# Optimization experiments

Measured on AMD Instinct MI355X. Metric: run time of the kernel, lower is better.

## Reference

```python
import jax, jax.numpy as jnp
import numpy as np

DIM = 256
NH = 8
HD = DIM // NH          # 32
KD = HD // 2            # 16, attn_ratio=0.5
SCALE = KD ** -0.5
EPS = 1e-3              # BatchNorm2d eps=0.001
B, H, W = 8, 32, 32


def _bn(x, g, b, m, v):
    # inference-mode BatchNorm2d over channel axis 1 of NCHW
    inv = g / jnp.sqrt(v + EPS)
    return x * inv[None, :, None, None] + (b - m * inv)[None, :, None, None]


def setup_inputs() -> dict:
    key = jax.random.key(0)
    ks = jax.random.split(key, 16)
    h_out = DIM + 2 * NH * KD  # 512
    return {
        "x": jax.random.normal(ks[0], (B, DIM, H, W), jnp.float32),
        "qkv_w": jax.random.normal(ks[1], (h_out, DIM), jnp.float32) * 0.05,
        "qkv_g": jax.random.uniform(ks[2], (h_out,), jnp.float32, 0.5, 1.5),
        "qkv_b": jax.random.normal(ks[3], (h_out,), jnp.float32) * 0.1,
        "qkv_m": jax.random.normal(ks[4], (h_out,), jnp.float32) * 0.1,
        "qkv_v": jax.random.uniform(ks[5], (h_out,), jnp.float32, 0.5, 1.5),
        "pe_w": jax.random.normal(ks[6], (DIM, 1, 3, 3), jnp.float32) * 0.1,
        "pe_g": jax.random.uniform(ks[7], (DIM,), jnp.float32, 0.5, 1.5),
        "pe_b": jax.random.normal(ks[8], (DIM,), jnp.float32) * 0.1,
        "pe_m": jax.random.normal(ks[9], (DIM,), jnp.float32) * 0.1,
        "pe_v": jax.random.uniform(ks[10], (DIM,), jnp.float32, 0.5, 1.5),
        "proj_w": jax.random.normal(ks[11], (DIM, DIM), jnp.float32) * 0.05,
        "proj_g": jax.random.uniform(ks[12], (DIM,), jnp.float32, 0.5, 1.5),
        "proj_b": jax.random.normal(ks[13], (DIM,), jnp.float32) * 0.1,
        "proj_m": jax.random.normal(ks[14], (DIM,), jnp.float32) * 0.1,
        "proj_v": jax.random.uniform(ks[15], (DIM,), jnp.float32, 0.5, 1.5),
    }


def reference(x, qkv_w, qkv_g, qkv_b, qkv_m, qkv_v,
              pe_w, pe_g, pe_b, pe_m, pe_v,
              proj_w, proj_g, proj_b, proj_m, proj_v):
    b, c, h, w = x.shape
    n = h * w
    # qkv: 1x1 conv (no bias) + BN, act=Identity
    qkv = _bn(jnp.einsum('oc,bchw->bohw', qkv_w, x), qkv_g, qkv_b, qkv_m, qkv_v)
    qkv = qkv.reshape(b, NH, 2 * KD + HD, n)
    q, k, v = jnp.split(qkv, [KD, 2 * KD], axis=2)  # [b,nh,kd,n],[b,nh,kd,n],[b,nh,hd,n]
    # attn = q^T @ k * scale, softmax over keys (last dim)
    attn = jax.nn.softmax(jnp.einsum('bhkn,bhkm->bhnm', q, k) * SCALE, axis=-1)
    # v @ attn^T -> [b,nh,hd,n]
    out = jnp.einsum('bhdj,bhij->bhdi', v, attn).reshape(b, c, h, w)
    # depthwise 3x3 positional branch on v (reshaped to spatial)
    v_sp = v.reshape(b, c, h, w)
    pe = jax.lax.conv_general_dilated(v_sp, pe_w, window_strides=(1, 1),
                                      padding=((1, 1), (1, 1)),
                                      feature_group_count=c)
    pe = _bn(pe, pe_g, pe_b, pe_m, pe_v)
    x_attn = out + pe
    # final 1x1 projection + BN
    return _bn(jnp.einsum('oc,bchw->bohw', proj_w, x_attn),
               proj_g, proj_b, proj_m, proj_v)
```

## Files before the change

### kernel.cpp

```cpp
#include <hip/hip_runtime.h>
#include <hip/hip_bf16.h>

#define B_    8
#define DIM_  256
#define NH_   8
#define HD_   32
#define KD_   16
#define HOUT_ 512
#define N_    1024
#define SCALE_ 0.25f
#define EPS_  1e-3f

typedef unsigned short u16;
typedef __attribute__((ext_vector_type(8))) short short8;
typedef __attribute__((ext_vector_type(4))) float f32x4;

union H4 { uint2 u; u16 e[4]; };

__device__ __forceinline__ float b2f(u16 u) {
    union { unsigned int i; float f; } c;
    c.i = ((unsigned int)u) << 16;
    return c.f;
}

__device__ __forceinline__ u16 f2b(float f) {
    union { float f; unsigned int i; } c;
    c.f = f;
    unsigned int x = c.i;
    return (u16)((x + 0x7fffu + ((x >> 16) & 1u)) >> 16);
}

__global__ __launch_bounds__(256) void k_prep(
    const float* __restrict__ qw, const float* __restrict__ pw,
    const float* __restrict__ pew,
    const float* __restrict__ qg, const float* __restrict__ qb,
    const float* __restrict__ qm, const float* __restrict__ qv,
    const float* __restrict__ pg, const float* __restrict__ pb,
    const float* __restrict__ pm, const float* __restrict__ pv,
    const float* __restrict__ eg, const float* __restrict__ eb,
    const float* __restrict__ em, const float* __restrict__ ev,
    u16* __restrict__ wq_bf, u16* __restrict__ wp_bf,
    float2* __restrict__ bnq, float2* __restrict__ bnp,
    float* __restrict__ wpe, float* __restrict__ bnpe)
{
    int i = blockIdx.x * 256 + threadIdx.x;
    wq_bf[i] = f2b(qw[i]);
    if (i < 65536) wp_bf[i] = f2b(pw[i]);
    if (i < 512) {
        float inv = qg[i] / sqrtf(qv[i] + EPS_);
        bnq[i] = make_float2(inv, qb[i] - qm[i] * inv);
    } else if (i < 768) {
        int o = i - 512;
        float inv = pg[o] / sqrtf(pv[o] + EPS_);
        bnp[o] = make_float2(inv, pb[o] - pm[o] * inv);
    }
    if (i < 2304) {
        int c = i / 9;
        float inv = eg[c] / sqrtf(ev[c] + EPS_);
        wpe[i] = pew[i] * inv;
        if (i % 9 == 0) bnpe[c] = eb[c] - em[c] * inv;
    }
}

__global__ __launch_bounds__(256) void k_xt(
    const float* __restrict__ x, u16* __restrict__ xT)
{
    __shared__ float t_s[64][65];
    int blk = blockIdx.x;
    int nt = blk & 15, ct = (blk >> 4) & 3, b = blk >> 6;
    int t = threadIdx.x;
    int c0 = ct * 64, n0 = nt * 64;
    #pragma unroll
    for (int i = 0; i < 16; ++i) {
        int idx = i * 256 + t;
        int c = idx >> 6, n = idx & 63;
        t_s[n][c] = x[(size_t)(b * DIM_ + c0 + c) * N_ + n0 + n];
    }
    __syncthreads();
    #pragma unroll
    for (int i = 0; i < 16; ++i) {
        int idx = i * 256 + t;
        int n = idx >> 6, c = idx & 63;
        xT[(size_t)(b * N_ + n0 + n) * DIM_ + c0 + c] = f2b(t_s[n][c]);
    }
}

__global__ __launch_bounds__(256) void k_qkv(
    const u16* __restrict__ xT, const u16* __restrict__ wbf,
    const float2* __restrict__ bn, u16* __restrict__ qkv)
{
    int blk = blockIdx.x;
    int nb = blk & 7, ob = (blk >> 3) & 7, b = blk >> 6;
    int t = threadIdx.x;
    int wv_ = t >> 6, lane = t & 63, quad = lane >> 4, l16 = lane & 15;
    int o_base = ob * 64 + (wv_ & 1) * 32;
    int n_base = nb * 128 + (wv_ >> 1) * 64;

    f32x4 acc[2][4];
    #pragma unroll
    for (int ot = 0; ot < 2; ++ot)
        #pragma unroll
        for (int nt = 0; nt < 4; ++nt) acc[ot][nt] = (f32x4){0.f, 0.f, 0.f, 0.f};

    const u16* xb = xT + (size_t)b * N_ * DIM_;
    for (int c0 = 0; c0 < DIM_; c0 += 32) {
        short8 af[2];
        #pragma unroll
        for (int ot = 0; ot < 2; ++ot)
            af[ot] = *(const short8*)(wbf + (size_t)(o_base + ot * 16 + l16) * DIM_ + c0 + quad * 8);
        short8 bf[4];
        #pragma unroll
        for (int nt = 0; nt < 4; ++nt)
            bf[nt] = *(const short8*)(xb + (size_t)(n_base + nt * 16 + l16) * DIM_ + c0 + quad * 8);
        #pragma unroll
        for (int ot = 0; ot < 2; ++ot)
            #pragma unroll
            for (int nt = 0; nt < 4; ++nt)
                acc[ot][nt] = __builtin_amdgcn_mfma_f32_16x16x32_bf16(af[ot], bf[nt], acc[ot][nt], 0, 0, 0);
    }
    #pragma unroll
    for (int ot = 0; ot < 2; ++ot)
        #pragma unroll
        for (int r = 0; r < 4; ++r) {
            int o = o_base + ot * 16 + quad * 4 + r;
            float2 ib = bn[o];
            u16* dst = qkv + (size_t)(b * HOUT_ + o) * N_ + n_base + l16;
            #pragma unroll
            for (int nt = 0; nt < 4; ++nt)
                dst[nt * 16] = f2b(acc[ot][nt][r] * ib.x + ib.y);
        }
}

struct MainSmem { u16 k_t[256][24]; u16 p_s[4][16][80]; };
union  SmemU    { MainSmem m; float v_pe[128][33]; };

__global__ __launch_bounds__(256) void k_attn(
    const u16* __restrict__ qkv, const float* __restrict__ wpe,
    const float* __restrict__ bnpe, u16* __restrict__ xattnT)
{
    __shared__ SmemU su;
    __shared__ u16   q_t[64][24];
    __shared__ float o_s[4][32][17];

    int blk = blockIdx.x;
    int qb = blk & 15;
    int h  = (blk >> 4) & 7;
    int b  = blk >> 7;
    int t    = threadIdx.x;
    int wv_  = t >> 6;
    int lane = t & 63;
    int quad = lane >> 4;
    int l16  = lane & 15;
    const u16* base = qkv + (size_t)(b * HOUT_ + h * 64) * N_;

    {
        int q = t & 63, d4 = (t >> 6) * 4;
        H4 hh;
        #pragma unroll
        for (int i = 0; i < 4; ++i)
            hh.e[i] = f2b(b2f(base[(size_t)(d4 + i) * N_ + qb * 64 + q]) * SCALE_);
        *(uint2*)&q_t[q][d4] = hh.u;
    }
    __syncthreads();

    short8 qf = {0, 0, 0, 0, 0, 0, 0, 0};
    if (quad < 2) qf = *(const short8*)&q_t[wv_ * 16 + l16][quad * 8];

    f32x4 oa0 = {0.f, 0.f, 0.f, 0.f};
    f32x4 oa1 = {0.f, 0.f, 0.f, 0.f};
    float l_acc[4] = {0.f, 0.f, 0.f, 0.f};

    for (int ch = 0; ch < 4; ++ch) {
        int ch0 = ch * 256;
        __syncthreads();
        {
            #pragma unroll
            for (int d4 = 0; d4 < 16; d4 += 4) {
                H4 hh;
                #pragma unroll
                for (int i = 0; i < 4; ++i)
                    hh.e[i] = base[(size_t)(16 + d4 + i) * N_ + ch0 + t];
                *(uint2*)&su.m.k_t[t][d4] = hh.u;
            }
        }
        __syncthreads();

        for (int kt = 0; kt < 4; ++kt) {
            int key0 = ch0 + kt * 64;
            #pragma unroll
            for (int nt = 0; nt < 4; ++nt) {
                short8 kf = {0, 0, 0, 0, 0, 0, 0, 0};
                if (quad < 2) kf = *(const short8*)&su.m.k_t[kt * 64 + nt * 16 + l16][quad * 8];
                f32x4 zero = {0.f, 0.f, 0.f, 0.f};
                f32x4 s = __builtin_amdgcn_mfma_f32_16x16x32_bf16(qf, kf, zero, 0, 0, 0);
                #pragma unroll
                for (int r = 0; r < 4; ++r) {
                    float p = __expf(fminf(s[r], 80.f));
                    l_acc[r] += p;
                    su.m.p_s[wv_][quad * 4 + r][nt * 16 + l16] = f2b(p);
                }
            }
            #pragma unroll
            for (int kc = 0; kc < 2; ++kc) {
                short8 pf = *(const short8*)&su.m.p_s[wv_][l16][kc * 32 + quad * 8];
                {
                    const u16* vsrc = base + (size_t)(32 + l16) * N_ + key0 + kc * 32 + quad * 8;
                    oa0 = __builtin_amdgcn_mfma_f32_16x16x32_bf16(pf, *(const short8*)vsrc, oa0, 0, 0, 0);
                }
                {
                    const u16* vsrc = base + (size_t)(48 + l16) * N_ + key0 + kc * 32 + quad * 8;
                    oa1 = __builtin_amdgcn_mfma_f32_16x16x32_bf16(pf, *(const short8*)vsrc, oa1, 0, 0, 0);
                }
            }
        }
    }

    #pragma unroll
    for (int r = 0; r < 4; ++r) {
        float v = l_acc[r];
        v += __shfl_xor(v, 1);
        v += __shfl_xor(v, 2);
        v += __shfl_xor(v, 4);
        v += __shfl_xor(v, 8);
        l_acc[r] = v;
    }
    #pragma unroll
    for (int r = 0; r < 4; ++r) {
        o_s[wv_][l16][quad * 4 + r]      = oa0[r] / l_acc[r];
        o_s[wv_][16 + l16][quad * 4 + r] = oa1[r] / l_acc[r];
    }
    __syncthreads();

    {
        int ybase = qb * 2 - 1;
        #pragma unroll
        for (int i = 0; i < 16; ++i) {
            int idx = i * 256 + t;
            int d = idx >> 7, px = idx & 127;
            int y = ybase + (px >> 5);
            float v = 0.f;
            if (y >= 0 && y < 32)
                v = b2f(base[(size_t)(32 + d) * N_ + y * 32 + (px & 31)]);
            su.v_pe[px][d] = v;
        }
    }
    __syncthreads();

    {
        int d = t & 31, pxg = t >> 5;
        int c = h * 32 + d;
        float w9[9];
        #pragma unroll
        for (int k = 0; k < 9; ++k) w9[k] = wpe[c * 9 + k];
        float beta = bnpe[c];
        #pragma unroll
        for (int ii = 0; ii < 8; ++ii) {
            int pl = pxg * 8 + ii;
            int xx0 = pl & 31;
            float s = beta;
            #pragma unroll
            for (int dy = -1; dy <= 1; ++dy) {
                #pragma unroll
                for (int dx = -1; dx <= 1; ++dx) {
                    int xx = xx0 + dx;
                    if (xx < 0 || xx > 31) continue;
                    s += w9[(dy + 1) * 3 + (dx + 1)] * su.v_pe[pl + 32 + dy * 32 + dx][d];
                }
            }
            float o = o_s[pl >> 4][d][pl & 15];
            xattnT[(size_t)(b * N_ + qb * 64 + pl) * DIM_ + c] = f2b(o + s);
        }
    }
}

__global__ __launch_bounds__(256) void k_proj(
    const u16* __restrict__ xattnT, const u16* __restrict__ wbf,
    const float2* __restrict__ bn, float* __restrict__ out)
{
    int blk = blockIdx.x;
    int nb = blk & 7, ob = (blk >> 3) & 3, b = blk >> 5;
    int t = threadIdx.x;
    int wv_ = t >> 6, lane = t & 63, quad = lane >> 4, l16 = lane & 15;
    int o_base = ob * 64 + (wv_ & 1) * 32;
    int n_base = nb * 128 + (wv_ >> 1) * 64;

    f32x4 acc[2][4];
    #pragma unroll
    for (int ot = 0; ot < 2; ++ot)
        #pragma unroll
        for (int nt = 0; nt < 4; ++nt) acc[ot][nt] = (f32x4){0.f, 0.f, 0.f, 0.f};

    const u16* xb = xattnT + (size_t)b * N_ * DIM_;
    for (int c0 = 0; c0 < DIM_; c0 += 32) {
        short8 af[2];
        #pragma unroll
        for (int ot = 0; ot < 2; ++ot)
            af[ot] = *(const short8*)(wbf + (size_t)(o_base + ot * 16 + l16) * DIM_ + c0 + quad * 8);
        short8 bf[4];
        #pragma unroll
        for (int nt = 0; nt < 4; ++nt)
            bf[nt] = *(const short8*)(xb + (size_t)(n_base + nt * 16 + l16) * DIM_ + c0 + quad * 8);
        #pragma unroll
        for (int ot = 0; ot < 2; ++ot)
            #pragma unroll
            for (int nt = 0; nt < 4; ++nt)
                acc[ot][nt] = __builtin_amdgcn_mfma_f32_16x16x32_bf16(af[ot], bf[nt], acc[ot][nt], 0, 0, 0);
    }
    #pragma unroll
    for (int ot = 0; ot < 2; ++ot)
        #pragma unroll
        for (int r = 0; r < 4; ++r) {
            int o = o_base + ot * 16 + quad * 4 + r;
            float2 ib = bn[o];
            float* dst = out + (size_t)(b * DIM_ + o) * N_ + n_base + l16;
            #pragma unroll
            for (int nt = 0; nt < 4; ++nt)
                dst[nt * 16] = acc[ot][nt][r] * ib.x + ib.y;
        }
}

extern "C" void kernel_launch(void* const* d_in, const int* in_sizes, int n_in,
                              void* d_out, int out_size, void* d_ws, size_t ws_size,
                              hipStream_t stream)
{
    const float* x      = (const float*)d_in[0];
    const float* qkv_w  = (const float*)d_in[1];
    const float* qkv_g  = (const float*)d_in[2];
    const float* qkv_b  = (const float*)d_in[3];
    const float* qkv_m  = (const float*)d_in[4];
    const float* qkv_v  = (const float*)d_in[5];
    const float* pe_w   = (const float*)d_in[6];
    const float* pe_g   = (const float*)d_in[7];
    const float* pe_b   = (const float*)d_in[8];
    const float* pe_m   = (const float*)d_in[9];
    const float* pe_v   = (const float*)d_in[10];
    const float* proj_w = (const float*)d_in[11];
    const float* proj_g = (const float*)d_in[12];
    const float* proj_b = (const float*)d_in[13];
    const float* proj_m = (const float*)d_in[14];
    const float* proj_v = (const float*)d_in[15];
    float* out = (float*)d_out;

    char* p = (char*)d_ws;
    u16*    qkv    = (u16*)p;    p += (size_t)B_ * HOUT_ * N_ * sizeof(u16);
    u16*    xT     = (u16*)p;    p += (size_t)B_ * N_ * DIM_ * sizeof(u16);
    u16*    xattnT = (u16*)p;    p += (size_t)B_ * N_ * DIM_ * sizeof(u16);
    u16*    wq_bf  = (u16*)p;    p += (size_t)HOUT_ * DIM_ * sizeof(u16);
    u16*    wp_bf  = (u16*)p;    p += (size_t)DIM_ * DIM_ * sizeof(u16);
    float2* bnq    = (float2*)p; p += 512 * sizeof(float2);
    float2* bnp    = (float2*)p; p += 256 * sizeof(float2);
    float*  wpe    = (float*)p;  p += 2304 * sizeof(float);
    float*  bnpe   = (float*)p;

    hipLaunchKernelGGL(k_prep, dim3(512), dim3(256), 0, stream,
                       qkv_w, proj_w, pe_w,
                       qkv_g, qkv_b, qkv_m, qkv_v,
                       proj_g, proj_b, proj_m, proj_v,
                       pe_g, pe_b, pe_m, pe_v,
                       wq_bf, wp_bf, bnq, bnp, wpe, bnpe);
    hipLaunchKernelGGL(k_xt, dim3(512), dim3(256), 0, stream, x, xT);
    hipLaunchKernelGGL(k_qkv, dim3(512), dim3(256), 0, stream,
                       xT, wq_bf, bnq, qkv);
    hipLaunchKernelGGL(k_attn, dim3(B_ * NH_ * 16), dim3(256), 0, stream,
                       qkv, wpe, bnpe, xattnT);
    hipLaunchKernelGGL(k_proj, dim3(256), dim3(256), 0, stream,
                       xattnT, wp_bf, bnp, out);
}
```

Before: 159.5 us.

## Rework attention with 32x32 MFMA and register P, fuse prep kernels, retile proj

Attention now computes S^T with 32x32x16 MFMAs and keeps P in registers, exchanging halves across the wave with a lane shuffle instead of staging through LDS. The four waves are split into two key halves and two query tiles, and the partial outputs and row sums are merged in shared memory in the epilogue. This removes the wasted half-K 16x16 MFMA and the LDS round trip for P. The prep and transpose kernels are merged into one launch, and the projection uses smaller tiles for twice as many blocks. Partial outputs are rounded to bf16 before the merge, which costs some precision.

After: 152.1 us. 1.05x faster.

```diff
diff --git a/kernel.cpp b/kernel.cpp
--- a/kernel.cpp
+++ b/kernel.cpp
@@ -12,10 +12,13 @@
 #define EPS_  1e-3f
 
 typedef unsigned short u16;
-typedef __attribute__((ext_vector_type(8))) short short8;
-typedef __attribute__((ext_vector_type(4))) float f32x4;
+typedef unsigned int   u32;
+typedef __attribute__((ext_vector_type(8)))  short short8;
+typedef __attribute__((ext_vector_type(4)))  float f32x4;
+typedef __attribute__((ext_vector_type(16))) float f32x16;
 
 union H4 { uint2 u; u16 e[4]; };
+union FragU { uint4 u; short8 s; };
 
 __device__ __forceinline__ float b2f(u16 u) {
     union { unsigned int i; float f; } c;
@@ -30,7 +33,8 @@
     return (u16)((x + 0x7fffu + ((x >> 16) & 1u)) >> 16);
 }
 
-__global__ __launch_bounds__(256) void k_prep(
+__global__ __launch_bounds__(256) void k_pre(
+    const float* __restrict__ x, u16* __restrict__ xT,
     const float* __restrict__ qw, const float* __restrict__ pw,
     const float* __restrict__ pew,
     const float* __restrict__ qg, const float* __restrict__ qb,
@@ -43,32 +47,30 @@
     float2* __restrict__ bnq, float2* __restrict__ bnp,
     float* __restrict__ wpe, float* __restrict__ bnpe)
 {
-    int i = blockIdx.x * 256 + threadIdx.x;
-    wq_bf[i] = f2b(qw[i]);
-    if (i < 65536) wp_bf[i] = f2b(pw[i]);
-    if (i < 512) {
-        float inv = qg[i] / sqrtf(qv[i] + EPS_);
-        bnq[i] = make_float2(inv, qb[i] - qm[i] * inv);
-    } else if (i < 768) {
-        int o = i - 512;
-        float inv = pg[o] / sqrtf(pv[o] + EPS_);
-        bnp[o] = make_float2(inv, pb[o] - pm[o] * inv);
-    }
-    if (i < 2304) {
-        int c = i / 9;
-        float inv = eg[c] / sqrtf(ev[c] + EPS_);
-        wpe[i] = pew[i] * inv;
-        if (i % 9 == 0) bnpe[c] = eb[c] - em[c] * inv;
-    }
-}
-
-__global__ __launch_bounds__(256) void k_xt(
-    const float* __restrict__ x, u16* __restrict__ xT)
-{
     __shared__ float t_s[64][65];
     int blk = blockIdx.x;
+    int t = threadIdx.x;
+    if (blk >= 512) {
+        int i = (blk - 512) * 256 + t;
+        wq_bf[i] = f2b(qw[i]);
+        if (i < 65536) wp_bf[i] = f2b(pw[i]);
+        if (i < 512) {
+            float inv = qg[i] / sqrtf(qv[i] + EPS_);
+            bnq[i] = make_float2(inv, qb[i] - qm[i] * inv);
+        } else if (i < 768) {
+            int o = i - 512;
+            float inv = pg[o] / sqrtf(pv[o] + EPS_);
+            bnp[o] = make_float2(inv, pb[o] - pm[o] * inv);
+        }
+        if (i < 2304) {
+            int c = i / 9;
+            float inv = eg[c] / sqrtf(ev[c] + EPS_);
+            wpe[i] = pew[i] * inv;
+            if (i % 9 == 0) bnpe[c] = eb[c] - em[c] * inv;
+        }
+        return;
+    }
     int nt = blk & 15, ct = (blk >> 4) & 3, b = blk >> 6;
-    int t = threadIdx.x;
     int c0 = ct * 64, n0 = nt * 64;
     #pragma unroll
     for (int i = 0; i < 16; ++i) {
@@ -131,17 +133,15 @@
         }
 }
 
-struct MainSmem { u16 k_t[256][24]; u16 p_s[4][16][80]; };
-union  SmemU    { MainSmem m; float v_pe[128][33]; };
+struct MainS { u16 q_t[64][24]; u16 k_t[2][256][24]; };
+struct EpiS  { u16 o_acc[2][32][66]; float l_s[2][64]; float v_pe[128][33]; };
+union  SmemU { MainS m; EpiS e; };
 
 __global__ __launch_bounds__(256) void k_attn(
     const u16* __restrict__ qkv, const float* __restrict__ wpe,
     const float* __restrict__ bnpe, u16* __restrict__ xattnT)
 {
     __shared__ SmemU su;
-    __shared__ u16   q_t[64][24];
-    __shared__ float o_s[4][32][17];
-
     int blk = blockIdx.x;
     int qb = blk & 15;
     int h  = (blk >> 4) & 7;
@@ -149,88 +149,90 @@
     int t    = threadIdx.x;
     int wv_  = t >> 6;
     int lane = t & 63;
-    int quad = lane >> 4;
-    int l16  = lane & 15;
+    int q5   = lane & 31;
+    int hw   = lane >> 5;
+    int kh   = wv_ >> 1;
+    int qt   = wv_ & 1;
     const u16* base = qkv + (size_t)(b * HOUT_ + h * 64) * N_;
+    int q0g = qb * 64;
 
     {
         int q = t & 63, d4 = (t >> 6) * 4;
         H4 hh;
         #pragma unroll
         for (int i = 0; i < 4; ++i)
-            hh.e[i] = f2b(b2f(base[(size_t)(d4 + i) * N_ + qb * 64 + q]) * SCALE_);
-        *(uint2*)&q_t[q][d4] = hh.u;
+            hh.e[i] = f2b(b2f(base[(size_t)(d4 + i) * N_ + q0g + q]) * SCALE_);
+        *(uint2*)&su.m.q_t[q][d4] = hh.u;
     }
     __syncthreads();
 
-    short8 qf = {0, 0, 0, 0, 0, 0, 0, 0};
-    if (quad < 2) qf = *(const short8*)&q_t[wv_ * 16 + l16][quad * 8];
-
-    f32x4 oa0 = {0.f, 0.f, 0.f, 0.f};
-    f32x4 oa1 = {0.f, 0.f, 0.f, 0.f};
-    float l_acc[4] = {0.f, 0.f, 0.f, 0.f};
-
-    for (int ch = 0; ch < 4; ++ch) {
-        int ch0 = ch * 256;
+    short8 qf = *(const short8*)&su.m.q_t[qt * 32 + q5][hw * 8];
+
+    f32x16 oacc = {0.f,0.f,0.f,0.f, 0.f,0.f,0.f,0.f, 0.f,0.f,0.f,0.f, 0.f,0.f,0.f,0.f};
+    float l_lane = 0.f;
+
+    for (int ch = 0; ch < 2; ++ch) {
         __syncthreads();
         {
             #pragma unroll
-            for (int d4 = 0; d4 < 16; d4 += 4) {
-                H4 hh;
+            for (int s2 = 0; s2 < 2; ++s2) {
+                int key = s2 * 512 + ch * 256 + t;
                 #pragma unroll
-                for (int i = 0; i < 4; ++i)
-                    hh.e[i] = base[(size_t)(16 + d4 + i) * N_ + ch0 + t];
-                *(uint2*)&su.m.k_t[t][d4] = hh.u;
-            }
-        }
-        __syncthreads();
-
-        for (int kt = 0; kt < 4; ++kt) {
-            int key0 = ch0 + kt * 64;
-            #pragma unroll
-            for (int nt = 0; nt < 4; ++nt) {
-                short8 kf = {0, 0, 0, 0, 0, 0, 0, 0};
-                if (quad < 2) kf = *(const short8*)&su.m.k_t[kt * 64 + nt * 16 + l16][quad * 8];
-                f32x4 zero = {0.f, 0.f, 0.f, 0.f};
-                f32x4 s = __builtin_amdgcn_mfma_f32_16x16x32_bf16(qf, kf, zero, 0, 0, 0);
-                #pragma unroll
-                for (int r = 0; r < 4; ++r) {
-                    float p = __expf(fminf(s[r], 80.f));
-                    l_acc[r] += p;
-                    su.m.p_s[wv_][quad * 4 + r][nt * 16 + l16] = f2b(p);
+                for (int d4 = 0; d4 < 16; d4 += 4) {
+                    H4 hh;
+                    #pragma unroll
+                    for (int i = 0; i < 4; ++i)
+                        hh.e[i] = base[(size_t)(16 + d4 + i) * N_ + key];
+                    *(uint2*)&su.m.k_t[s2][t][d4] = hh.u;
                 }
             }
-            #pragma unroll
-            for (int kc = 0; kc < 2; ++kc) {
-                short8 pf = *(const short8*)&su.m.p_s[wv_][l16][kc * 32 + quad * 8];
-                {
-                    const u16* vsrc = base + (size_t)(32 + l16) * N_ + key0 + kc * 32 + quad * 8;
-                    oa0 = __builtin_amdgcn_mfma_f32_16x16x32_bf16(pf, *(const short8*)vsrc, oa0, 0, 0, 0);
-                }
-                {
-                    const u16* vsrc = base + (size_t)(48 + l16) * N_ + key0 + kc * 32 + quad * 8;
-                    oa1 = __builtin_amdgcn_mfma_f32_16x16x32_bf16(pf, *(const short8*)vsrc, oa1, 0, 0, 0);
-                }
+        }
+        __syncthreads();
+
+        #pragma unroll 2
+        for (int tile = 0; tile < 8; ++tile) {
+            int key0 = kh * 512 + ch * 256 + tile * 32;
+            short8 kf = *(const short8*)&su.m.k_t[kh][tile * 32 + q5][hw * 8];
+            f32x16 z = {0.f,0.f,0.f,0.f, 0.f,0.f,0.f,0.f, 0.f,0.f,0.f,0.f, 0.f,0.f,0.f,0.f};
+            f32x16 sT = __builtin_amdgcn_mfma_f32_32x32x16_bf16(kf, qf, z, 0, 0, 0);
+            u32 pk[8];
+            #pragma unroll
+            for (int j = 0; j < 8; ++j) {
+                float p0 = __expf(fminf(sT[2 * j], 80.f));
+                float p1 = __expf(fminf(sT[2 * j + 1], 80.f));
+                l_lane += p0 + p1;
+                pk[j] = (u32)f2b(p0) | ((u32)f2b(p1) << 16);
             }
-        }
-    }
-
-    #pragma unroll
-    for (int r = 0; r < 4; ++r) {
-        float v = l_acc[r];
-        v += __shfl_xor(v, 1);
-        v += __shfl_xor(v, 2);
-        v += __shfl_xor(v, 4);
-        v += __shfl_xor(v, 8);
-        l_acc[r] = v;
-    }
-    #pragma unroll
-    for (int r = 0; r < 4; ++r) {
-        o_s[wv_][l16][quad * 4 + r]      = oa0[r] / l_acc[r];
-        o_s[wv_][16 + l16][quad * 4 + r] = oa1[r] / l_acc[r];
-    }
+            #pragma unroll
+            for (int s = 0; s < 2; ++s) {
+                u32 s0 = hw ? pk[4 * s + 0] : pk[4 * s + 2];
+                u32 s1 = hw ? pk[4 * s + 1] : pk[4 * s + 3];
+                u32 r0 = __shfl_xor(s0, 32);
+                u32 r1 = __shfl_xor(s1, 32);
+                FragU pf;
+                pf.u.x = hw ? r0 : pk[4 * s + 0];
+                pf.u.y = hw ? r1 : pk[4 * s + 1];
+                pf.u.z = hw ? pk[4 * s + 2] : r0;
+                pf.u.w = hw ? pk[4 * s + 3] : r1;
+                const u16* vsrc = base + (size_t)(32 + q5) * N_ + key0 + s * 16 + hw * 8;
+                short8 vf = *(const short8*)vsrc;
+                oacc = __builtin_amdgcn_mfma_f32_32x32x16_bf16(vf, pf.s, oacc, 0, 0, 0);
+            }
+        }
+    }
+
+    float l_q = l_lane + __shfl_xor(l_lane, 32);
     __syncthreads();
 
+    {
+        int qg = qt * 32 + q5;
+        #pragma unroll
+        for (int r = 0; r < 16; ++r) {
+            int d = (r & 3) + 8 * (r >> 2) + 4 * hw;
+            su.e.o_acc[kh][d][qg] = f2b(oacc[r]);
+        }
+        if (hw == 0) su.e.l_s[kh][qg] = l_q;
+    }
     {
         int ybase = qb * 2 - 1;
         #pragma unroll
@@ -241,7 +243,7 @@
             float v = 0.f;
             if (y >= 0 && y < 32)
                 v = b2f(base[(size_t)(32 + d) * N_ + y * 32 + (px & 31)]);
-            su.v_pe[px][d] = v;
+            su.e.v_pe[px][d] = v;
         }
     }
     __syncthreads();
@@ -264,11 +266,12 @@
                 for (int dx = -1; dx <= 1; ++dx) {
                     int xx = xx0 + dx;
                     if (xx < 0 || xx > 31) continue;
-                    s += w9[(dy + 1) * 3 + (dx + 1)] * su.v_pe[pl + 32 + dy * 32 + dx][d];
+                    s += w9[(dy + 1) * 3 + (dx + 1)] * su.e.v_pe[pl + 32 + dy * 32 + dx][d];
                 }
             }
-            float o = o_s[pl >> 4][d][pl & 15];
-            xattnT[(size_t)(b * N_ + qb * 64 + pl) * DIM_ + c] = f2b(o + s);
+            float o = b2f(su.e.o_acc[0][d][pl]) + b2f(su.e.o_acc[1][d][pl]);
+            float l = su.e.l_s[0][pl] + su.e.l_s[1][pl];
+            xattnT[(size_t)(b * N_ + q0g + pl) * DIM_ + c] = f2b(o / fmaxf(l, 1e-30f) + s);
         }
     }
 }
@@ -278,17 +281,17 @@
     const float2* __restrict__ bn, float* __restrict__ out)
 {
     int blk = blockIdx.x;
-    int nb = blk & 7, ob = (blk >> 3) & 3, b = blk >> 5;
+    int nb = blk & 15, ob = (blk >> 4) & 3, b = blk >> 6;
     int t = threadIdx.x;
     int wv_ = t >> 6, lane = t & 63, quad = lane >> 4, l16 = lane & 15;
     int o_base = ob * 64 + (wv_ & 1) * 32;
-    int n_base = nb * 128 + (wv_ >> 1) * 64;
-
-    f32x4 acc[2][4];
+    int n_base = nb * 64 + (wv_ >> 1) * 32;
+
+    f32x4 acc[2][2];
     #pragma unroll
     for (int ot = 0; ot < 2; ++ot)
         #pragma unroll
-        for (int nt = 0; nt < 4; ++nt) acc[ot][nt] = (f32x4){0.f, 0.f, 0.f, 0.f};
+        for (int nt = 0; nt < 2; ++nt) acc[ot][nt] = (f32x4){0.f, 0.f, 0.f, 0.f};
 
     const u16* xb = xattnT + (size_t)b * N_ * DIM_;
     for (int c0 = 0; c0 < DIM_; c0 += 32) {
@@ -296,14 +299,14 @@
         #pragma unroll
         for (int ot = 0; ot < 2; ++ot)
             af[ot] = *(const short8*)(wbf + (size_t)(o_base + ot * 16 + l16) * DIM_ + c0 + quad * 8);
-        short8 bf[4];
-        #pragma unroll
-        for (int nt = 0; nt < 4; ++nt)
+        short8 bf[2];
+        #pragma unroll
+        for (int nt = 0; nt < 2; ++nt)
             bf[nt] = *(const short8*)(xb + (size_t)(n_base + nt * 16 + l16) * DIM_ + c0 + quad * 8);
         #pragma unroll
         for (int ot = 0; ot < 2; ++ot)
             #pragma unroll
-            for (int nt = 0; nt < 4; ++nt)
+            for (int nt = 0; nt < 2; ++nt)
                 acc[ot][nt] = __builtin_amdgcn_mfma_f32_16x16x32_bf16(af[ot], bf[nt], acc[ot][nt], 0, 0, 0);
     }
     #pragma unroll
@@ -314,7 +317,7 @@
             float2 ib = bn[o];
             float* dst = out + (size_t)(b * DIM_ + o) * N_ + n_base + l16;
             #pragma unroll
-            for (int nt = 0; nt < 4; ++nt)
+            for (int nt = 0; nt < 2; ++nt)
                 dst[nt * 16] = acc[ot][nt][r] * ib.x + ib.y;
         }
 }
@@ -352,17 +355,16 @@
     float*  wpe    = (float*)p;  p += 2304 * sizeof(float);
     float*  bnpe   = (float*)p;
 
-    hipLaunchKernelGGL(k_prep, dim3(512), dim3(256), 0, stream,
-                       qkv_w, proj_w, pe_w,
+    hipLaunchKernelGGL(k_pre, dim3(1024), dim3(256), 0, stream,
+                       x, xT, qkv_w, proj_w, pe_w,
                        qkv_g, qkv_b, qkv_m, qkv_v,
                        proj_g, proj_b, proj_m, proj_v,
                        pe_g, pe_b, pe_m, pe_v,
                        wq_bf, wp_bf, bnq, bnp, wpe, bnpe);
-    hipLaunchKernelGGL(k_xt, dim3(512), dim3(256), 0, stream, x, xT);
     hipLaunchKernelGGL(k_qkv, dim3(512), dim3(256), 0, stream,
                        xT, wq_bf, bnq, qkv);
-    hipLaunchKernelGGL(k_attn, dim3(B_ * NH_ * 16), dim3(256), 0, stream,
+    hipLaunchKernelGGL(k_attn, dim3(1024), dim3(256), 0, stream,
                        qkv, wpe, bnpe, xattnT);
-    hipLaunchKernelGGL(k_proj, dim3(256), dim3(256), 0, stream,
+    hipLaunchKernelGGL(k_proj, dim3(512), dim3(256), 0, stream,
                        xattnT, wp_bf, bnp, out);
 }
```
